# Kernel tuning notes

Hardware: AMD Instinct MI355X
Metric: run time of the kernel (lower is better)

## Reference

```python
import jax, jax.numpy as jnp
import numpy as np

B, S, H, K = 4, 2048, 1024, 4
DT, TAU_MIN, TAU_MAX = 0.1, 1.0, 5.0
SCALE = 0.01
LN_EPS = 1e-5


def setup_inputs() -> dict:
    key = jax.random.key(0)
    ks = jax.random.split(key, 8)
    inv = 1.0 / np.sqrt(H)
    return {
        "hidden_states": jax.random.normal(ks[0], (B, S, H), dtype=jnp.float32),
        "conv_w": jax.random.normal(ks[1], (H, K), dtype=jnp.float32) * 0.25,  # depthwise causal conv weights
        "W_rec": jax.random.normal(ks[2], (H, H), dtype=jnp.float32) * inv,    # Linear(H,H,bias=False).weight
        "tau_w1": jax.random.normal(ks[3], (2 * H, H // 2), dtype=jnp.float32) * (1.0 / np.sqrt(2 * H)),
        "tau_b1": jnp.zeros((H // 2,), dtype=jnp.float32),
        "tau_w2": jax.random.normal(ks[4], (H // 2, 1), dtype=jnp.float32) * (1.0 / np.sqrt(H // 2)),
        "tau_b2": jnp.zeros((1,), dtype=jnp.float32),
        "ln_g": jnp.ones((H,), dtype=jnp.float32),
        "ln_b": jnp.zeros((H,), dtype=jnp.float32),
    }


def _shortconv(x, conv_w):
    # depthwise causal conv over seq: x [B,S,H], conv_w [H,K]
    xp = jnp.pad(x, ((0, 0), (K - 1, 0), (0, 0)))
    out = jnp.zeros_like(x)
    for k in range(K):  # K=4, static small loop
        out = out + conv_w[None, None, :, k] * xp[:, k:k + x.shape[1], :]
    return out


def _liquid(x, W_rec, tau_w1, tau_b1, tau_w2, tau_b2, ln_g, ln_b):
    # x: [B,S,H] -> per-step gated recurrence with LayerNorm, via lax.scan
    def step(h, x_t):
        combined = jnp.concatenate([x_t, h], axis=-1)                  # [B,2H]
        tau_raw = jax.nn.sigmoid(
            jnp.tanh(combined @ tau_w1 + tau_b1) @ tau_w2 + tau_b2)    # [B,1]
        tau = TAU_MIN + (TAU_MAX - TAU_MIN) * tau_raw
        f_xh = jnp.tanh(x_t + h @ W_rec.T)                             # [B,H]
        h = h + DT * (-h + f_xh) / tau
        mu = jnp.mean(h, axis=-1, keepdims=True)
        var = jnp.mean((h - mu) ** 2, axis=-1, keepdims=True)
        h = (h - mu) / jnp.sqrt(var + LN_EPS) * ln_g + ln_b            # LayerNorm
        return h, h

    h0 = jnp.zeros((x.shape[0], H), dtype=x.dtype)
    _, liq = jax.lax.scan(step, h0, jnp.swapaxes(x, 0, 1))             # liq [S,B,H]
    return jnp.swapaxes(liq, 0, 1)


def reference(hidden_states, conv_w, W_rec, tau_w1, tau_b1, tau_w2, tau_b2, ln_g, ln_b):
    sc = _shortconv(hidden_states, conv_w)
    liq = _liquid(hidden_states, W_rec, tau_w1, tau_b1, tau_w2, tau_b2, ln_g, ln_b)
    return sc + SCALE * (liq - sc)
```

## Files before the change

kernel.cpp:

```cpp
#include <hip/hip_runtime.h>
#include <math.h>

#define SS   2048
#define HH   1024
#define HHF  512
#define NWG  192
#define REC_WGS 128
#define NTH  256
#define NCNT 16

__device__ __forceinline__ float dot4f(float4 a, float4 b){
  return a.x*b.x + a.y*b.y + a.z*b.z + a.w*b.w;
}

__device__ __forceinline__ float2 aload2(const float* p){
  unsigned long long v = __hip_atomic_load((const unsigned long long*)p,
                                           __ATOMIC_RELAXED, __HIP_MEMORY_SCOPE_AGENT);
  union { unsigned long long u; float2 f; } c; c.u = v; return c.f;
}
__device__ __forceinline__ void astore1(float* p, float v){
  __hip_atomic_store(p, v, __ATOMIC_RELAXED, __HIP_MEMORY_SCOPE_AGENT);
}
__device__ __forceinline__ float aload1(const float* p){
  return __hip_atomic_load(p, __ATOMIC_RELAXED, __HIP_MEMORY_SCOPE_AGENT);
}
__device__ __forceinline__ unsigned uload(const unsigned* p){
  return __hip_atomic_load(p, __ATOMIC_RELAXED, __HIP_MEMORY_SCOPE_AGENT);
}

__global__ __launch_bounds__(256) void transpose_w1h(const float* __restrict__ tw1,
                                                     float* __restrict__ w1hT){
  __shared__ float ts[32][33];
  int c  = threadIdx.x & 31;
  int r4 = (threadIdx.x >> 5) * 4;
  int bi = blockIdx.x * 32;
  int bm = blockIdx.y * 32;
  #pragma unroll
  for (int rr = 0; rr < 4; ++rr)
    ts[r4+rr][c] = tw1[(size_t)(1024 + bi + r4 + rr) * 512 + bm + c];
  __syncthreads();
  #pragma unroll
  for (int rr = 0; rr < 4; ++rr)
    w1hT[(size_t)(bm + r4 + rr) * 1024 + bi + c] = ts[c][r4+rr];
}

__global__ __launch_bounds__(256) void gemm_xtau(const float* __restrict__ X,
                                                 const float* __restrict__ tw1,
                                                 const float* __restrict__ b1,
                                                 float* __restrict__ xtau){
  __shared__ float Xs[16][68];
  __shared__ float Ws[16][68];
  const int tid = threadIdx.x;
  const int tx = tid & 15, ty = tid >> 4;
  const int rowbase = blockIdx.y * 64;
  const int colbase = blockIdx.x * 64;
  const int xr  = tid >> 2,  xk4 = (tid & 3) * 4;
  const int wr  = tid >> 4,  wc4 = (tid & 15) * 4;
  float acc[4][4];
  #pragma unroll
  for (int i=0;i<4;++i){
    #pragma unroll
    for (int j=0;j<4;++j) acc[i][j]=0.f;
  }
  for (int k0 = 0; k0 < 1024; k0 += 16){
    float4 xv = *(const float4*)&X  [(size_t)(rowbase + xr)*1024 + k0 + xk4];
    float4 wv = *(const float4*)&tw1[(size_t)(k0 + wr)*512 + colbase + wc4];
    __syncthreads();
    Xs[xk4+0][xr]=xv.x; Xs[xk4+1][xr]=xv.y; Xs[xk4+2][xr]=xv.z; Xs[xk4+3][xr]=xv.w;
    *(float4*)&Ws[wr][wc4] = wv;
    __syncthreads();
    #pragma unroll
    for (int kk=0;kk<16;++kk){
      float4 av = *(const float4*)&Xs[kk][ty*4];
      float4 bv = *(const float4*)&Ws[kk][tx*4];
      acc[0][0]+=av.x*bv.x; acc[0][1]+=av.x*bv.y; acc[0][2]+=av.x*bv.z; acc[0][3]+=av.x*bv.w;
      acc[1][0]+=av.y*bv.x; acc[1][1]+=av.y*bv.y; acc[1][2]+=av.y*bv.z; acc[1][3]+=av.y*bv.w;
      acc[2][0]+=av.z*bv.x; acc[2][1]+=av.z*bv.y; acc[2][2]+=av.z*bv.z; acc[2][3]+=av.z*bv.w;
      acc[3][0]+=av.w*bv.x; acc[3][1]+=av.w*bv.y; acc[3][2]+=av.w*bv.z; acc[3][3]+=av.w*bv.w;
    }
  }
  float4 bias = *(const float4*)&b1[colbase + tx*4];
  #pragma unroll
  for (int i=0;i<4;++i){
    float4 o;
    o.x=acc[i][0]+bias.x; o.y=acc[i][1]+bias.y; o.z=acc[i][2]+bias.z; o.w=acc[i][3]+bias.w;
    *(float4*)&xtau[(size_t)(rowbase + ty*4 + i)*512 + colbase + tx*4] = o;
  }
}

__global__ __launch_bounds__(256, 1) void liquid_kernel(
    const float* __restrict__ X, const float* __restrict__ Wrec,
    const float* __restrict__ w1hT, const float* __restrict__ tw2,
    const float* __restrict__ tb2, const float* __restrict__ lng,
    const float* __restrict__ lnb, const float* __restrict__ xtau,
    unsigned* __restrict__ cnt, float* __restrict__ fbuf,
    float* __restrict__ taup, float* __restrict__ out)
{
  __shared__ float hs[2][4][1024];

  const int tid  = threadIdx.x;
  const int wv   = tid >> 6;
  const int lane = tid & 63;
  const int wg   = blockIdx.x;

  for (int p = tid; p < 8192; p += NTH) (&hs[0][0][0])[p] = 0.f;

  float4 wreg[2][4];
  #pragma unroll
  for (int rr = 0; rr < 2; ++rr){
    const float* wrow = (wg < REC_WGS)
        ? (Wrec + (size_t)(wg*8 + wv*2 + rr)*1024)
        : (w1hT + (size_t)((wg - REC_WGS)*8 + wv*2 + rr)*1024);
    #pragma unroll
    for (int k = 0; k < 4; ++k)
      wreg[rr][k] = *(const float4*)&wrow[4*lane + 256*k];
  }
  float4 g4[4], be4[4];
  #pragma unroll
  for (int k = 0; k < 4; ++k){
    g4[k]  = *(const float4*)&lng[4*lane + 256*k];
    be4[k] = *(const float4*)&lnb[4*lane + 256*k];
  }
  const float b2 = tb2[0];
  float w2r0 = 0.f, w2r1 = 0.f;
  if (wg >= REC_WGS){
    w2r0 = tw2[(wg - REC_WGS)*8 + wv*2 + 0];
    w2r1 = tw2[(wg - REC_WGS)*8 + wv*2 + 1];
  }
  __syncthreads();

  for (int t = 0; t < SS; ++t){
    const int cur = t & 1, nxt = cur ^ 1;

    float xpre = 0.f;
    if (lane < 8){
      const int rr = lane >> 2, b = lane & 3;
      if (wg < REC_WGS)
        xpre = X[((size_t)b*SS + t)*HH + wg*8 + wv*2 + rr];
      else
        xpre = xtau[((size_t)b*SS + t)*HHF + (wg - REC_WGS)*8 + wv*2 + rr];
    }

    float acc[8];
    #pragma unroll
    for (int a=0;a<8;++a) acc[a]=0.f;
    #pragma unroll
    for (int k=0;k<4;++k){
      const int off = 4*lane + 256*k;
      float4 h0 = *(const float4*)&hs[cur][0][off];
      float4 h1 = *(const float4*)&hs[cur][1][off];
      float4 h2 = *(const float4*)&hs[cur][2][off];
      float4 h3 = *(const float4*)&hs[cur][3][off];
      #pragma unroll
      for (int rr=0;rr<2;++rr){
        acc[rr*4+0] += dot4f(wreg[rr][k], h0);
        acc[rr*4+1] += dot4f(wreg[rr][k], h1);
        acc[rr*4+2] += dot4f(wreg[rr][k], h2);
        acc[rr*4+3] += dot4f(wreg[rr][k], h3);
      }
    }
    #pragma unroll
    for (int a=0;a<8;++a){
      float v = acc[a];
      #pragma unroll
      for (int o=32;o>0;o>>=1) v += __shfl_xor(v, o, 64);
      acc[a]=v;
    }
    float sel = acc[0];
    sel = (lane==1)?acc[1]:sel; sel = (lane==2)?acc[2]:sel;
    sel = (lane==3)?acc[3]:sel; sel = (lane==4)?acc[4]:sel;
    sel = (lane==5)?acc[5]:sel; sel = (lane==6)?acc[6]:sel;
    sel = (lane==7)?acc[7]:sel;
    float fval = tanhf(xpre + sel);

    if (wg < REC_WGS){
      if (lane < 8)
        astore1(&fbuf[cur*4096 + (lane&3)*1024 + wg*8 + wv*2 + (lane>>2)], fval);
    } else {
      float w2s = (lane & 4) ? w2r1 : w2r0;
      float contrib = fval * w2s;
      contrib += __shfl_xor(contrib, 4, 64);
      if (lane < 4)
        astore1(&taup[cur*1024 + lane*256 + (wg - REC_WGS)*4 + wv], contrib);
    }

    __syncthreads();
    if (tid == 0)
      __hip_atomic_fetch_add(&cnt[(wg & (NCNT-1))*16], 1u,
                             __ATOMIC_RELAXED, __HIP_MEMORY_SCOPE_AGENT);

    if (wv == 0 && lane < NCNT){
      const unsigned tgt = (unsigned)NWG * (unsigned)(t + 1);
      int guard = 0;
      while (true){
        unsigned s = uload(&cnt[lane*16]);
        #pragma unroll
        for (int o=8;o>0;o>>=1) s += (unsigned)__shfl_xor((int)s, o, 64);
        if (s >= tgt) break;
        __builtin_amdgcn_s_sleep(1);
        if (++guard > 100000) break;
      }
    }
    __syncthreads();

    const float* fb = fbuf + cur*4096 + wv*1024;
    float2 pr[8]; float tv[4];
    #pragma unroll
    for (int q=0;q<8;++q)
      pr[q] = aload2(&fb[(q>>1)*256 + 4*lane + (q&1)*2]);
    #pragma unroll
    for (int j=0;j<4;++j)
      tv[j] = aload1(&taup[cur*1024 + wv*256 + lane + 64*j]);

    float tpart = tv[0] + tv[1] + tv[2] + tv[3];
    #pragma unroll
    for (int o=32;o>0;o>>=1) tpart += __shfl_xor(tpart, o, 64);
    float pre = tpart + b2;
    float sig = 1.f / (1.f + expf(-pre));
    float al  = 0.1f / (1.f + 4.f*sig);

    float s1 = 0.f, s2 = 0.f;
    float4 hp4[4];
    #pragma unroll
    for (int k=0;k<4;++k){
      const int off = 4*lane + 256*k;
      float4 h4 = *(const float4*)&hs[cur][wv][off];
      float4 hp;
      hp.x = h4.x + al*(pr[2*k  ].x - h4.x);
      hp.y = h4.y + al*(pr[2*k  ].y - h4.y);
      hp.z = h4.z + al*(pr[2*k+1].x - h4.z);
      hp.w = h4.w + al*(pr[2*k+1].y - h4.w);
      hp4[k] = hp;
      s1 += hp.x + hp.y + hp.z + hp.w;
      s2 += hp.x*hp.x + hp.y*hp.y + hp.z*hp.z + hp.w*hp.w;
    }
    #pragma unroll
    for (int o=32;o>0;o>>=1){
      s1 += __shfl_xor(s1, o, 64);
      s2 += __shfl_xor(s2, o, 64);
    }
    float mu   = s1 * (1.f/1024.f);
    float var  = s2 * (1.f/1024.f) - mu*mu;
    float rstd = rsqrtf(var + 1e-5f);
    #pragma unroll
    for (int k=0;k<4;++k){
      const int off = 4*lane + 256*k;
      float4 hp = hp4[k];
      float4 o4;
      o4.x = (hp.x - mu)*rstd*g4[k].x + be4[k].x;
      o4.y = (hp.y - mu)*rstd*g4[k].y + be4[k].y;
      o4.z = (hp.z - mu)*rstd*g4[k].z + be4[k].z;
      o4.w = (hp.w - mu)*rstd*g4[k].w + be4[k].w;
      *(float4*)&hs[nxt][wv][off] = o4;
      if (wg < 16 && (wg >> 2) == k && (lane >> 4) == (wg & 3))
        *(float4*)&out[((size_t)wv*SS + t)*HH + off] = o4;
    }

    asm volatile("s_waitcnt lgkmcnt(0)" ::: "memory");
    __builtin_amdgcn_sched_barrier(0);
    __builtin_amdgcn_s_barrier();
  }
}

__global__ __launch_bounds__(256) void finalize_kernel(const float* __restrict__ X,
                                                       const float* __restrict__ cw,
                                                       float* __restrict__ out){
  size_t gid = (size_t)blockIdx.x * 256 + threadIdx.x;
  size_t gi  = gid * 4;
  int b   = (int)(gi >> 21);
  int rem = (int)(gi & 2097151);
  int t   = rem >> 10;
  int i   = rem & 1023;
  float4 l4 = *(const float4*)&out[gi];
  const float* xb = X + ((size_t)b*SS)*HH + i;
  float4 z4 = make_float4(0.f,0.f,0.f,0.f);
  float4 xk0 = (t >= 3) ? *(const float4*)&xb[(size_t)(t-3)*HH] : z4;
  float4 xk1 = (t >= 2) ? *(const float4*)&xb[(size_t)(t-2)*HH] : z4;
  float4 xk2 = (t >= 1) ? *(const float4*)&xb[(size_t)(t-1)*HH] : z4;
  float4 xk3 =            *(const float4*)&xb[(size_t)t*HH];
  float4 cw0 = *(const float4*)&cw[(i+0)*4];
  float4 cw1 = *(const float4*)&cw[(i+1)*4];
  float4 cw2 = *(const float4*)&cw[(i+2)*4];
  float4 cw3 = *(const float4*)&cw[(i+3)*4];
  float4 sc;
  sc.x = cw0.x*xk0.x + cw0.y*xk1.x + cw0.z*xk2.x + cw0.w*xk3.x;
  sc.y = cw1.x*xk0.y + cw1.y*xk1.y + cw1.z*xk2.y + cw1.w*xk3.y;
  sc.z = cw2.x*xk0.z + cw2.y*xk1.z + cw2.z*xk2.z + cw2.w*xk3.z;
  sc.w = cw3.x*xk0.w + cw3.y*xk1.w + cw3.z*xk2.w + cw3.w*xk3.w;
  float4 o;
  o.x = sc.x + 0.01f*(l4.x - sc.x);
  o.y = sc.y + 0.01f*(l4.y - sc.y);
  o.z = sc.z + 0.01f*(l4.z - sc.z);
  o.w = sc.w + 0.01f*(l4.w - sc.w);
  *(float4*)&out[gi] = o;
}

extern "C" void kernel_launch(void* const* d_in, const int* in_sizes, int n_in,
                              void* d_out, int out_size, void* d_ws, size_t ws_size,
                              hipStream_t stream) {
  const float* X     = (const float*)d_in[0];
  const float* convw = (const float*)d_in[1];
  const float* Wrec  = (const float*)d_in[2];
  const float* tw1   = (const float*)d_in[3];
  const float* tb1   = (const float*)d_in[4];
  const float* tw2   = (const float*)d_in[5];
  const float* tb2   = (const float*)d_in[6];
  const float* lng   = (const float*)d_in[7];
  const float* lnb   = (const float*)d_in[8];
  float* out = (float*)d_out;
  float* wsf = (float*)d_ws;

  unsigned* cnt = (unsigned*)d_ws;
  float* fbuf = wsf + 256;
  float* taup = wsf + 8448;
  float* w1hT = wsf + 10496;
  float* xtau = w1hT + 512*1024;

  hipMemsetAsync(d_ws, 0, 1024, stream);
  transpose_w1h<<<dim3(32,16), dim3(256), 0, stream>>>(tw1, w1hT);
  gemm_xtau   <<<dim3(8,128),  dim3(256), 0, stream>>>(X, tw1, tb1, xtau);
  liquid_kernel<<<dim3(NWG),   dim3(NTH), 0, stream>>>(X, Wrec, w1hT, tw2, tb2,
                                                       lng, lnb, xtau, cnt, fbuf,
                                                       taup, out);
  finalize_kernel<<<dim3(8192), dim3(256), 0, stream>>>(X, convw, out);
}
```

Baseline: 10.14 ms.

## Split recurrence across batch into independent 48-workgroup groups with per-batch barriers

Each batch element now gets its own group of 48 workgroups (32 computing W_rec rows, 16 computing tau hidden rows), each holding 8 weight rows per wave in registers. Grid-wide synchronisation becomes a per-batch barrier over 48 workgroups, and the spin loop drops its sleep. Each workgroup keeps only one hidden state and computes LayerNorm over it with a cross-wave LDS reduction. This removes the 192-workgroup global barrier and the 4x redundant LayerNorm work, at the cost of four times the weight registers per thread (occupancy/spill risk) and weights being replicated four times across groups.

Measured after the change: 10.03 ms. About the same (-1.1%).

```diff
diff --git a/kernel.cpp b/kernel.cpp
--- a/kernel.cpp
+++ b/kernel.cpp
@@ -5,9 +5,9 @@
 #define HH   1024
 #define HHF  512
 #define NWG  192
-#define REC_WGS 128
+#define DWG  48
+#define RECWG 32
 #define NTH  256
-#define NCNT 16
 
 __device__ __forceinline__ float dot4f(float4 a, float4 b){
   return a.x*b.x + a.y*b.y + a.z*b.z + a.w*b.w;
@@ -96,37 +96,33 @@
     unsigned* __restrict__ cnt, float* __restrict__ fbuf,
     float* __restrict__ taup, float* __restrict__ out)
 {
-  __shared__ float hs[2][4][1024];
+  __shared__ float hs[2][1024];
+  __shared__ float stats_lds[8];
 
   const int tid  = threadIdx.x;
   const int wv   = tid >> 6;
   const int lane = tid & 63;
-  const int wg   = blockIdx.x;
-
-  for (int p = tid; p < 8192; p += NTH) (&hs[0][0][0])[p] = 0.f;
-
-  float4 wreg[2][4];
-  #pragma unroll
-  for (int rr = 0; rr < 2; ++rr){
-    const float* wrow = (wg < REC_WGS)
-        ? (Wrec + (size_t)(wg*8 + wv*2 + rr)*1024)
-        : (w1hT + (size_t)((wg - REC_WGS)*8 + wv*2 + rr)*1024);
+  const int d     = blockIdx.x & 3;
+  const int local = blockIdx.x >> 2;
+
+  for (int p = tid; p < 2048; p += NTH) (&hs[0][0])[p] = 0.f;
+
+  const bool isrec = (local < RECWG);
+  const int base = isrec ? (local*32 + wv*8) : ((local - RECWG)*32 + wv*8);
+  float4 wreg[8][4];
+  #pragma unroll
+  for (int rr = 0; rr < 8; ++rr){
+    const float* wrow = isrec ? (Wrec + (size_t)(base + rr)*1024)
+                              : (w1hT + (size_t)(base + rr)*1024);
     #pragma unroll
     for (int k = 0; k < 4; ++k)
       wreg[rr][k] = *(const float4*)&wrow[4*lane + 256*k];
   }
-  float4 g4[4], be4[4];
-  #pragma unroll
-  for (int k = 0; k < 4; ++k){
-    g4[k]  = *(const float4*)&lng[4*lane + 256*k];
-    be4[k] = *(const float4*)&lnb[4*lane + 256*k];
-  }
+  float4 g4 = *(const float4*)&lng[4*tid];
+  float4 be4 = *(const float4*)&lnb[4*tid];
   const float b2 = tb2[0];
-  float w2r0 = 0.f, w2r1 = 0.f;
-  if (wg >= REC_WGS){
-    w2r0 = tw2[(wg - REC_WGS)*8 + wv*2 + 0];
-    w2r1 = tw2[(wg - REC_WGS)*8 + wv*2 + 1];
-  }
+  float w2r = 0.f;
+  if (!isrec && lane < 8) w2r = tw2[base + lane];
   __syncthreads();
 
   for (int t = 0; t < SS; ++t){
@@ -134,11 +130,8 @@
 
     float xpre = 0.f;
     if (lane < 8){
-      const int rr = lane >> 2, b = lane & 3;
-      if (wg < REC_WGS)
-        xpre = X[((size_t)b*SS + t)*HH + wg*8 + wv*2 + rr];
-      else
-        xpre = xtau[((size_t)b*SS + t)*HHF + (wg - REC_WGS)*8 + wv*2 + rr];
+      xpre = isrec ? X   [((size_t)d*SS + t)*HH  + base + lane]
+                   : xtau[((size_t)d*SS + t)*HHF + base + lane];
     }
 
     float acc[8];
@@ -146,18 +139,9 @@
     for (int a=0;a<8;++a) acc[a]=0.f;
     #pragma unroll
     for (int k=0;k<4;++k){
-      const int off = 4*lane + 256*k;
-      float4 h0 = *(const float4*)&hs[cur][0][off];
-      float4 h1 = *(const float4*)&hs[cur][1][off];
-      float4 h2 = *(const float4*)&hs[cur][2][off];
-      float4 h3 = *(const float4*)&hs[cur][3][off];
+      float4 h4 = *(const float4*)&hs[cur][4*lane + 256*k];
       #pragma unroll
-      for (int rr=0;rr<2;++rr){
-        acc[rr*4+0] += dot4f(wreg[rr][k], h0);
-        acc[rr*4+1] += dot4f(wreg[rr][k], h1);
-        acc[rr*4+2] += dot4f(wreg[rr][k], h2);
-        acc[rr*4+3] += dot4f(wreg[rr][k], h3);
-      }
+      for (int rr=0;rr<8;++rr) acc[rr] += dot4f(wreg[rr][k], h4);
     }
     #pragma unroll
     for (int a=0;a<8;++a){
@@ -173,88 +157,74 @@
     sel = (lane==7)?acc[7]:sel;
     float fval = tanhf(xpre + sel);
 
-    if (wg < REC_WGS){
+    if (isrec){
       if (lane < 8)
-        astore1(&fbuf[cur*4096 + (lane&3)*1024 + wg*8 + wv*2 + (lane>>2)], fval);
+        astore1(&fbuf[cur*4096 + d*1024 + base + lane], fval);
     } else {
-      float w2s = (lane & 4) ? w2r1 : w2r0;
-      float contrib = fval * w2s;
-      contrib += __shfl_xor(contrib, 4, 64);
-      if (lane < 4)
-        astore1(&taup[cur*1024 + lane*256 + (wg - REC_WGS)*4 + wv], contrib);
+      float contrib = (lane < 8) ? fval * w2r : 0.f;
+      contrib += __shfl_xor(contrib, 1, 8);
+      contrib += __shfl_xor(contrib, 2, 8);
+      contrib += __shfl_xor(contrib, 4, 8);
+      if (lane == 0)
+        astore1(&taup[cur*256 + d*64 + (local - RECWG)*4 + wv], contrib);
     }
 
     __syncthreads();
     if (tid == 0)
-      __hip_atomic_fetch_add(&cnt[(wg & (NCNT-1))*16], 1u,
+      __hip_atomic_fetch_add(&cnt[(d*4 + (local & 3))*16], 1u,
                              __ATOMIC_RELAXED, __HIP_MEMORY_SCOPE_AGENT);
 
-    if (wv == 0 && lane < NCNT){
-      const unsigned tgt = (unsigned)NWG * (unsigned)(t + 1);
+    if (tid == 0){
+      const unsigned tgt = (unsigned)DWG * (unsigned)(t + 1);
       int guard = 0;
-      while (true){
-        unsigned s = uload(&cnt[lane*16]);
-        #pragma unroll
-        for (int o=8;o>0;o>>=1) s += (unsigned)__shfl_xor((int)s, o, 64);
+      while (guard < 50000){
+        unsigned s = uload(&cnt[(d*4 + 0)*16])
+                   + uload(&cnt[(d*4 + 1)*16])
+                   + uload(&cnt[(d*4 + 2)*16])
+                   + uload(&cnt[(d*4 + 3)*16]);
         if (s >= tgt) break;
-        __builtin_amdgcn_s_sleep(1);
-        if (++guard > 100000) break;
+        ++guard;
       }
     }
     __syncthreads();
 
-    const float* fb = fbuf + cur*4096 + wv*1024;
-    float2 pr[8]; float tv[4];
-    #pragma unroll
-    for (int q=0;q<8;++q)
-      pr[q] = aload2(&fb[(q>>1)*256 + 4*lane + (q&1)*2]);
-    #pragma unroll
-    for (int j=0;j<4;++j)
-      tv[j] = aload1(&taup[cur*1024 + wv*256 + lane + 64*j]);
-
-    float tpart = tv[0] + tv[1] + tv[2] + tv[3];
+    const float* fb = fbuf + cur*4096 + d*1024 + 4*tid;
+    float2 lo = aload2(fb);
+    float2 hi = aload2(fb + 2);
+    float tpart = aload1(&taup[cur*256 + d*64 + lane]);
     #pragma unroll
     for (int o=32;o>0;o>>=1) tpart += __shfl_xor(tpart, o, 64);
-    float pre = tpart + b2;
-    float sig = 1.f / (1.f + expf(-pre));
-    float al  = 0.1f / (1.f + 4.f*sig);
-
-    float s1 = 0.f, s2 = 0.f;
-    float4 hp4[4];
-    #pragma unroll
-    for (int k=0;k<4;++k){
-      const int off = 4*lane + 256*k;
-      float4 h4 = *(const float4*)&hs[cur][wv][off];
-      float4 hp;
-      hp.x = h4.x + al*(pr[2*k  ].x - h4.x);
-      hp.y = h4.y + al*(pr[2*k  ].y - h4.y);
-      hp.z = h4.z + al*(pr[2*k+1].x - h4.z);
-      hp.w = h4.w + al*(pr[2*k+1].y - h4.w);
-      hp4[k] = hp;
-      s1 += hp.x + hp.y + hp.z + hp.w;
-      s2 += hp.x*hp.x + hp.y*hp.y + hp.z*hp.z + hp.w*hp.w;
-    }
+    const float sig = 1.f / (1.f + expf(-(tpart + b2)));
+    const float al  = 0.1f / (1.f + 4.f*sig);
+
+    float4 h4 = *(const float4*)&hs[cur][4*tid];
+    float4 hp;
+    hp.x = h4.x + al*(lo.x - h4.x);
+    hp.y = h4.y + al*(lo.y - h4.y);
+    hp.z = h4.z + al*(hi.x - h4.z);
+    hp.w = h4.w + al*(hi.y - h4.w);
+    float s1 = hp.x + hp.y + hp.z + hp.w;
+    float s2 = hp.x*hp.x + hp.y*hp.y + hp.z*hp.z + hp.w*hp.w;
     #pragma unroll
     for (int o=32;o>0;o>>=1){
       s1 += __shfl_xor(s1, o, 64);
       s2 += __shfl_xor(s2, o, 64);
     }
-    float mu   = s1 * (1.f/1024.f);
-    float var  = s2 * (1.f/1024.f) - mu*mu;
-    float rstd = rsqrtf(var + 1e-5f);
-    #pragma unroll
-    for (int k=0;k<4;++k){
-      const int off = 4*lane + 256*k;
-      float4 hp = hp4[k];
-      float4 o4;
-      o4.x = (hp.x - mu)*rstd*g4[k].x + be4[k].x;
-      o4.y = (hp.y - mu)*rstd*g4[k].y + be4[k].y;
-      o4.z = (hp.z - mu)*rstd*g4[k].z + be4[k].z;
-      o4.w = (hp.w - mu)*rstd*g4[k].w + be4[k].w;
-      *(float4*)&hs[nxt][wv][off] = o4;
-      if (wg < 16 && (wg >> 2) == k && (lane >> 4) == (wg & 3))
-        *(float4*)&out[((size_t)wv*SS + t)*HH + off] = o4;
-    }
+    if (lane == 0){ stats_lds[wv*2] = s1; stats_lds[wv*2+1] = s2; }
+    __syncthreads();
+    const float s1t = stats_lds[0] + stats_lds[2] + stats_lds[4] + stats_lds[6];
+    const float s2t = stats_lds[1] + stats_lds[3] + stats_lds[5] + stats_lds[7];
+    const float mu   = s1t * (1.f/1024.f);
+    const float var  = s2t * (1.f/1024.f) - mu*mu;
+    const float rstd = rsqrtf(var + 1e-5f);
+    float4 o4;
+    o4.x = (hp.x - mu)*rstd*g4.x + be4.x;
+    o4.y = (hp.y - mu)*rstd*g4.y + be4.y;
+    o4.z = (hp.z - mu)*rstd*g4.z + be4.z;
+    o4.w = (hp.w - mu)*rstd*g4.w + be4.w;
+    *(float4*)&hs[nxt][4*tid] = o4;
+    if (local == 0)
+      *(float4*)&out[((size_t)d*SS + t)*HH + 4*tid] = o4;
 
     asm volatile("s_waitcnt lgkmcnt(0)" ::: "memory");
     __builtin_amdgcn_sched_barrier(0);
@@ -313,7 +283,7 @@
   unsigned* cnt = (unsigned*)d_ws;
   float* fbuf = wsf + 256;
   float* taup = wsf + 8448;
-  float* w1hT = wsf + 10496;
+  float* w1hT = wsf + 8960;
   float* xtau = w1hT + 512*1024;
 
   hipMemsetAsync(d_ws, 0, 1024, stream);
```
